# Optimization experiments

Measured on AMD Instinct MI355X. Metric: run time of the kernel, lower is better.

Reference implementation:

```python
import jax, jax.numpy as jnp
import numpy as np

B, NQ, NK, H = 4, 2048, 2048, 512
TEMP = 1.0


def setup_inputs() -> dict:
    key = jax.random.key(0)
    ks = jax.random.split(key, 13)
    s = 0.02
    inp = {
        "query_feat": jax.random.normal(ks[0], (B, NQ, H), jnp.float32),
        "key_feat": jax.random.normal(ks[1], (B, NK, H), jnp.float32),
        "qm_uncert": jax.random.normal(ks[2], (B, NQ), jnp.float32),
        "md_uncert": jax.random.normal(ks[3], (B, NK), jnp.float32),
        "Wq": jax.random.normal(ks[4], (H, H), jnp.float32) * s,
        "bq": jnp.zeros((H,), jnp.float32),
        "Wk": jax.random.normal(ks[5], (H, H), jnp.float32) * s,
        "bk": jnp.zeros((H,), jnp.float32),
        "Wv": jax.random.normal(ks[6], (H, H), jnp.float32) * s,
        "bv": jnp.zeros((H,), jnp.float32),
        "Wo": jax.random.normal(ks[7], (H, H), jnp.float32) * s,
        "bo": jnp.zeros((H,), jnp.float32),
        "tau": jnp.float32(1.0),
    }
    return inp


def reference(query_feat, key_feat, qm_uncert, md_uncert,
              Wq, bq, Wk, bk, Wv, bv, Wo, bo, tau):
    h = query_feat.shape[-1]
    Q = query_feat @ Wq.T + bq          # [B,Nq,H]
    K = key_feat @ Wk.T + bk            # [B,Nk,H]
    V = key_feat @ Wv.T + bv            # [B,Nk,H]

    # scaled dot-product logits
    logits = jnp.einsum('bqh,bkh->bqk', Q, K) / jnp.sqrt(jnp.asarray(h, logits_dtype(Q)))

    # uncertainty weight: sigmoid(tau * (qm_i + md_j)), then sanitize (mult mode)
    u = jax.nn.sigmoid(tau * (qm_uncert[:, :, None] + md_uncert[:, None, :]))
    u = jnp.nan_to_num(u, nan=1.0, posinf=1e6, neginf=1e-6)
    u = jnp.clip(u, 1e-6, 1e6)
    row_sum = jnp.sum(jnp.abs(u), axis=-1, keepdims=True)
    u = jnp.where(row_sum <= 1e-12, jnp.asarray(1e-6, u.dtype), u)

    logits = (logits * u) / TEMP

    # rows fully masked to -1e9 get zeroed (no mask here, but kept for faithfulness)
    all_masked = jnp.all(logits == -1e9, axis=-1, keepdims=True)
    logits = jnp.where(all_masked, jnp.zeros_like(logits), logits)

    attn = jax.nn.softmax(logits, axis=-1)  # dropout p=0 -> identity
    att = jnp.einsum('bqk,bkh->bqh', attn, V)
    out = att @ Wo.T + bo
    return out, attn


def logits_dtype(x):
    return x.dtype
```

## Files before the change

kernel.cpp:

```cpp
#include <hip/hip_runtime.h>
#include <stdint.h>

#define DEVI static __device__ __forceinline__

typedef unsigned short u16;
typedef short bf16x8 __attribute__((ext_vector_type(8)));
typedef u16 u16x8 __attribute__((ext_vector_type(8)));
typedef u16 u16x4 __attribute__((ext_vector_type(4)));
typedef float f32x4 __attribute__((ext_vector_type(4)));

DEVI u16 f2bf(float f) {
    uint32_t u = __builtin_bit_cast(uint32_t, f);
    u += 0x7FFFu + ((u >> 16) & 1u);
    return (u16)(u >> 16);
}
DEVI float bf2f(u16 u) { return __builtin_bit_cast(float, (uint32_t)u << 16); }

struct GemmArgs {
    const void* A;
    const void* A2;
    long long aStrideBytes;
    int lda;
    const u16* Bm;
    long long bStrideElts;
    int ldb;
    int K;
    const float* bias; const float* bias2; const float* bias3;
    u16* outB;
    float* outF;
    long long outFStride;
    const float* qm; const float* md; const float* tauPtr; float scale;
    float* partials;
    u16* vt;
};

enum { EPI_PROJ = 0, EPI_PROJV = 1, EPI_LOGITS = 2, EPI_PV = 3, EPI_OUT = 4,
       EPI_LOGITSB = 5, EPI_PROJ3 = 6 };

template <int EPI, bool AF32>
__global__ __launch_bounds__(256, 2) void gemm_bt(GemmArgs p) {
    __shared__ u16 As[128 * 32];
    __shared__ u16 Bs[128 * 32];
    __shared__ float redBuf[2][128];

    const int tid = threadIdx.x;
    const int lane = tid & 63;
    const int wave = tid >> 6;
    const int g = lane >> 4, lr = lane & 15;
    const int wr = wave >> 1, wc = wave & 1;
    const int z = blockIdx.z;
    const int rowBase = blockIdx.x * 128;
    const int colBase = blockIdx.y * 128;

    int batch = z, koff = 0;
    if constexpr (EPI == EPI_PV) { batch = z & 3; koff = (z >> 2) * p.K; }

    const char* Abase;
    const u16* Bbase;
    const float* bias = p.bias;
    if constexpr (EPI == EPI_PROJ3) {
        Abase = (const char*)(z == 0 ? p.A : p.A2);
        Bbase = p.Bm + (size_t)z * 512 * 512;
        bias = (z == 0) ? p.bias : (z == 1 ? p.bias2 : p.bias3);
    } else {
        Abase = (const char*)p.A + (size_t)batch * p.aStrideBytes + (size_t)koff * (AF32 ? 4 : 2);
        Bbase = p.Bm + (size_t)batch * p.bStrideElts + koff;
    }

    f32x4 acc[4][4] = {};

    const int nk = p.K >> 5;
    for (int kt = 0; kt < nk; ++kt) {
        const int kb = kt << 5;
        float4 areg[4];
        if (AF32) {
            const float* Af = (const float*)Abase;
            const int arow = tid >> 1, kh = (tid & 1) << 4;
            const float* src = Af + (size_t)(rowBase + arow) * p.lda + kb + kh;
            #pragma unroll
            for (int j = 0; j < 4; ++j) areg[j] = ((const float4*)src)[j];
        }
        __syncthreads();
        if (AF32) {
            const int arow = tid >> 1, kh = (tid & 1) << 4;
            u16 tmp[16];
            #pragma unroll
            for (int j = 0; j < 4; ++j) {
                tmp[4 * j + 0] = f2bf(areg[j].x);
                tmp[4 * j + 1] = f2bf(areg[j].y);
                tmp[4 * j + 2] = f2bf(areg[j].z);
                tmp[4 * j + 3] = f2bf(areg[j].w);
            }
            #pragma unroll
            for (int h = 0; h < 2; ++h)
                *(u16x8*)&As[arow * 32 + kh + h * 8] = *(u16x8*)&tmp[h * 8];
        } else {
            #pragma unroll
            for (int i = 0; i < 2; ++i) {
                int c = i * 256 + tid;
                const u16* gp = (const u16*)Abase + (size_t)(rowBase + (c >> 2)) * p.lda + kb + (c & 3) * 8;
                char* lp = (char*)As + (i * 256 + wave * 64) * 16;
                __builtin_amdgcn_global_load_lds((const __attribute__((address_space(1))) void*)gp,
                                                 (__attribute__((address_space(3))) void*)lp, 16, 0, 0);
            }
        }
        #pragma unroll
        for (int i = 0; i < 2; ++i) {
            int c = i * 256 + tid;
            const u16* gp = Bbase + (size_t)(colBase + (c >> 2)) * p.ldb + kb + (c & 3) * 8;
            char* lp = (char*)Bs + (i * 256 + wave * 64) * 16;
            __builtin_amdgcn_global_load_lds((const __attribute__((address_space(1))) void*)gp,
                                             (__attribute__((address_space(3))) void*)lp, 16, 0, 0);
        }
        __syncthreads();

        bf16x8 af[4], bfr[4];
        #pragma unroll
        for (int m = 0; m < 4; ++m)
            af[m] = *(const bf16x8*)&As[(wr * 64 + m * 16 + lr) * 32 + g * 8];
        #pragma unroll
        for (int n = 0; n < 4; ++n)
            bfr[n] = *(const bf16x8*)&Bs[(wc * 64 + n * 16 + lr) * 32 + g * 8];
        #pragma unroll
        for (int m = 0; m < 4; ++m)
            #pragma unroll
            for (int n = 0; n < 4; ++n)
                acc[m][n] = __builtin_amdgcn_mfma_f32_16x16x32_bf16(af[m], bfr[n], acc[m][n], 0, 0, 0);
    }

    const int rB = rowBase + wr * 64;
    const int cB = colBase + wc * 64;

    if constexpr (EPI == EPI_PROJ || EPI == EPI_PROJ3) {
        if (EPI == EPI_PROJ || z < 2) {
            u16* dst = (EPI == EPI_PROJ3) ? p.outB + (size_t)z * 8192 * 512 : p.outB;
            #pragma unroll
            for (int n = 0; n < 4; ++n) {
                int col = cB + n * 16 + lr;
                float bv = bias[col];
                #pragma unroll
                for (int m = 0; m < 4; ++m) {
                    int r0 = rB + m * 16 + g * 4;
                    #pragma unroll
                    for (int i = 0; i < 4; ++i)
                        dst[(size_t)(r0 + i) * 512 + col] = f2bf(acc[m][n][i] + bv);
                }
            }
        } else {
            #pragma unroll
            for (int n = 0; n < 4; ++n) {
                int col = cB + n * 16 + lr;
                float bv = bias[col];
                #pragma unroll
                for (int m = 0; m < 4; ++m) {
                    int r0 = rB + m * 16 + g * 4;
                    int b = r0 >> 11, k0 = r0 & 2047;
                    u16x4 pk;
                    #pragma unroll
                    for (int i = 0; i < 4; ++i) pk[i] = f2bf(acc[m][n][i] + bv);
                    *(u16x4*)&p.vt[((size_t)b * 512 + col) * 2048 + k0] = pk;
                }
            }
        }
    } else if constexpr (EPI == EPI_LOGITS || EPI == EPI_LOGITSB) {
        const float* qmB = p.qm + z * 2048;
        const float* mdB = p.md + z * 2048;
        const float tau = *p.tauPtr;
        float* outRow = p.outF + (size_t)z * p.outFStride;
        float mdv[4];
        #pragma unroll
        for (int n = 0; n < 4; ++n) mdv[n] = mdB[cB + n * 16 + lr];
        #pragma unroll
        for (int m = 0; m < 4; ++m) {
            int r0 = rB + m * 16 + g * 4;
            #pragma unroll
            for (int i = 0; i < 4; ++i) {
                int q = r0 + i;
                float qv = qmB[q];
                float rs = 0.f;
                #pragma unroll
                for (int n = 0; n < 4; ++n) {
                    float t = tau * (qv + mdv[n]);
                    float u = 1.0f / (1.0f + __expf(-t));
                    u = fminf(fmaxf(u, 1e-6f), 1e6f);
                    float e = __expf(acc[m][n][i] * p.scale * u);
                    if (EPI == EPI_LOGITSB)
                        p.outB[((size_t)(z * 2048 + q)) * 2048 + cB + n * 16 + lr] = f2bf(e);
                    else
                        outRow[(size_t)q * 2048 + cB + n * 16 + lr] = e;
                    rs += e;
                }
                #pragma unroll
                for (int off = 1; off < 16; off <<= 1) rs += __shfl_xor(rs, off, 64);
                if (lr == 0) redBuf[wc][wr * 64 + m * 16 + g * 4 + i] = rs;
            }
        }
        __syncthreads();
        if (tid < 128) {
            float s = redBuf[0][tid] + redBuf[1][tid];
            int q = rowBase + tid;
            p.partials[((size_t)z * 2048 + q) * 16 + blockIdx.y] = s;
        }
    } else if constexpr (EPI == EPI_PV) {
        const int split = z >> 2;
        u16* dst = p.outB + (size_t)split * 8192 * 512;
        #pragma unroll
        for (int n = 0; n < 4; ++n) {
            int col = cB + n * 16 + lr;
            #pragma unroll
            for (int m = 0; m < 4; ++m) {
                int r0 = rB + m * 16 + g * 4;
                size_t gr = (size_t)batch * 2048 + r0;
                #pragma unroll
                for (int i = 0; i < 4; ++i)
                    dst[(gr + i) * 512 + col] = f2bf(acc[m][n][i]);
            }
        }
    } else {
        #pragma unroll
        for (int n = 0; n < 4; ++n) {
            int col = cB + n * 16 + lr;
            float bv = p.bias[col];
            #pragma unroll
            for (int m = 0; m < 4; ++m) {
                int r0 = rB + m * 16 + g * 4;
                #pragma unroll
                for (int i = 0; i < 4; ++i)
                    p.outF[(size_t)(r0 + i) * 512 + col] = acc[m][n][i] + bv;
            }
        }
    }
}

__global__ void cvt_weights(const float* a, const float* b, const float* c, const float* d,
                            u16* dst) {
    const float* src;
    switch (blockIdx.y) {
        case 0: src = a; break;
        case 1: src = b; break;
        case 2: src = c; break;
        default: src = d; break;
    }
    int i = (blockIdx.x * 256 + threadIdx.x) * 4;
    float4 v = *(const float4*)(src + i);
    u16x4 u = { f2bf(v.x), f2bf(v.y), f2bf(v.z), f2bf(v.w) };
    *(u16x4*)(dst + (size_t)blockIdx.y * 512 * 512 + i) = u;
}

__global__ void rowsum_inv(const float* __restrict__ partials, float* __restrict__ invs) {
    int r = blockIdx.x * 256 + threadIdx.x;
    float s = 0.f;
    #pragma unroll
    for (int t = 0; t < 16; ++t) s += partials[r * 16 + t];
    invs[r] = 1.0f / s;
}

__global__ void normalize_attn(float* __restrict__ attn, const float* __restrict__ invs) {
    size_t i4 = (size_t)blockIdx.x * 256 + threadIdx.x;
    int row = (int)(i4 >> 9);
    float s = invs[row];
    float4 v = ((const float4*)attn)[i4];
    v.x *= s; v.y *= s; v.z *= s; v.w *= s;
    ((float4*)attn)[i4] = v;
}

__global__ void normalize_bf(const u16* __restrict__ e, float* __restrict__ attn,
                             const float* __restrict__ invs) {
    size_t i8 = (size_t)blockIdx.x * 256 + threadIdx.x;
    size_t e0 = i8 * 8;
    int row = (int)(e0 >> 11);
    float s = invs[row];
    u16x8 v = *(const u16x8*)(e + e0);
    float4 a, b;
    a.x = bf2f(v[0]) * s; a.y = bf2f(v[1]) * s; a.z = bf2f(v[2]) * s; a.w = bf2f(v[3]) * s;
    b.x = bf2f(v[4]) * s; b.y = bf2f(v[5]) * s; b.z = bf2f(v[6]) * s; b.w = bf2f(v[7]) * s;
    ((float4*)(attn + e0))[0] = a;
    ((float4*)(attn + e0))[1] = b;
}

__global__ void pv_reduce(const u16* __restrict__ part, const float* __restrict__ invs,
                          u16* __restrict__ attB) {
    size_t i8 = (size_t)blockIdx.x * 256 + threadIdx.x;
    size_t e0 = i8 * 8;
    int row = (int)(e0 >> 9);
    float s = invs ? invs[row] : 1.0f;
    u16x8 p0 = *(const u16x8*)(part + e0);
    u16x8 p1 = *(const u16x8*)(part + (size_t)8192 * 512 + e0);
    u16x8 o;
    #pragma unroll
    for (int j = 0; j < 8; ++j) o[j] = f2bf((bf2f(p0[j]) + bf2f(p1[j])) * s);
    *(u16x8*)(attB + e0) = o;
}

extern "C" void kernel_launch(void* const* d_in, const int* in_sizes, int n_in,
                              void* d_out, int out_size, void* d_ws, size_t ws_size,
                              hipStream_t stream) {
    const float* qf  = (const float*)d_in[0];
    const float* kf  = (const float*)d_in[1];
    const float* qm  = (const float*)d_in[2];
    const float* md  = (const float*)d_in[3];
    const float* Wq  = (const float*)d_in[4];
    const float* bq  = (const float*)d_in[5];
    const float* Wk  = (const float*)d_in[6];
    const float* bk  = (const float*)d_in[7];
    const float* Wv  = (const float*)d_in[8];
    const float* bv  = (const float*)d_in[9];
    const float* Wo  = (const float*)d_in[10];
    const float* bo  = (const float*)d_in[11];
    const float* tau = (const float*)d_in[12];

    float* out  = (float*)d_out;
    float* attn = out + (size_t)4 * 2048 * 512;

    const size_t NV = (size_t)8192 * 512;
    u16* Qb   = (u16*)d_ws;
    u16* Kb   = Qb + NV;
    u16* Vtb  = Kb + NV;
    u16* Wqb  = Vtb + NV;
    u16* Wob  = Wqb + (size_t)3 * 512 * 512;
    float* partials = (float*)(Wqb + (size_t)4 * 512 * 512);
    float* invs = partials + (size_t)8192 * 16;
    u16* attE = (u16*)(invs + 8192);
    size_t need = (size_t)((char*)(attE + (size_t)4 * 2048 * 2048) - (char*)d_ws);
    const bool big = ws_size >= need;

    u16* partialPV = Qb;
    u16* attB = Vtb;

    dim3 blk(256);
    cvt_weights<<<dim3(256, 4), blk, 0, stream>>>(Wq, Wk, Wv, Wo, Wqb);

    GemmArgs a = {};
    a.A = qf; a.A2 = kf; a.lda = 512; a.ldb = 512; a.K = 512;
    a.Bm = Wqb; a.bias = bq; a.bias2 = bk; a.bias3 = bv;
    a.outB = Qb; a.vt = Vtb;
    gemm_bt<EPI_PROJ3, true><<<dim3(64, 4, 3), blk, 0, stream>>>(a);

    GemmArgs lg = {};
    lg.A = Qb; lg.aStrideBytes = (long long)2048 * 512 * 2; lg.lda = 512;
    lg.Bm = Kb; lg.bStrideElts = (long long)2048 * 512; lg.ldb = 512;
    lg.K = 512;
    lg.qm = qm; lg.md = md; lg.tauPtr = tau;
    lg.scale = 0.04419417382415922f;
    lg.partials = partials;
    if (big) {
        lg.outB = attE;
        gemm_bt<EPI_LOGITSB, false><<<dim3(16, 16, 4), blk, 0, stream>>>(lg);
    } else {
        lg.outF = attn; lg.outFStride = (long long)2048 * 2048;
        gemm_bt<EPI_LOGITS, false><<<dim3(16, 16, 4), blk, 0, stream>>>(lg);
    }

    rowsum_inv<<<dim3(32), blk, 0, stream>>>(partials, invs);

    if (big)
        normalize_bf<<<dim3(8192), blk, 0, stream>>>(attE, attn, invs);
    else
        normalize_attn<<<dim3(16384), blk, 0, stream>>>(attn, invs);

    GemmArgs pv = {};
    pv.Bm = Vtb; pv.bStrideElts = (long long)512 * 2048; pv.ldb = 2048;
    pv.K = 1024; pv.outB = partialPV; pv.lda = 2048;
    if (big) {
        pv.A = attE; pv.aStrideBytes = (long long)2048 * 2048 * 2;
        gemm_bt<EPI_PV, false><<<dim3(16, 4, 8), blk, 0, stream>>>(pv);
        pv_reduce<<<dim3(2048), blk, 0, stream>>>(partialPV, invs, attB);
    } else {
        pv.A = attn; pv.aStrideBytes = (long long)2048 * 2048 * 4;
        gemm_bt<EPI_PV, true><<<dim3(16, 4, 8), blk, 0, stream>>>(pv);
        pv_reduce<<<dim3(2048), blk, 0, stream>>>(partialPV, nullptr, attB);
    }

    GemmArgs og = {};
    og.A = attB; og.lda = 512;
    og.Bm = Wob; og.ldb = 512;
    og.K = 512; og.bias = bo; og.outF = out;
    gemm_bt<EPI_OUT, false><<<dim3(64, 4, 1), blk, 0, stream>>>(og);
}
```

Baseline: 143.3 us.

## Fuse attn normalization into PV grid and split-K reduction into output GEMM

Removes the separate normalize_bf and pv_reduce kernels. The bf16-to-fp32 normalized attention write is done by extra blocks (blockIdx.y==4) inside the PV GEMM launch, so it runs alongside the matmul. The output projection now loads both split-K partial PV buffers, sums and scales them by the inverse row sum while staging A into LDS, and uses a 64-row tile to keep the grid larger. This saves two launches and one round trip of the intermediate through memory, at the cost of heavier A staging in the output GEMM and uneven work across blocks in the PV grid.

```diff
diff --git a/kernel.cpp b/kernel.cpp
--- a/kernel.cpp
+++ b/kernel.cpp
@@ -31,15 +31,16 @@
     long long outFStride;
     const float* qm; const float* md; const float* tauPtr; float scale;
     float* partials;
+    const float* invsPtr;
     u16* vt;
 };
 
-enum { EPI_PROJ = 0, EPI_PROJV = 1, EPI_LOGITS = 2, EPI_PV = 3, EPI_OUT = 4,
-       EPI_LOGITSB = 5, EPI_PROJ3 = 6 };
-
-template <int EPI, bool AF32>
+enum { EPI_PROJ3 = 0, EPI_LOGITS = 1, EPI_LOGITSB = 2, EPI_PV = 3, EPI_OUT = 4 };
+
+template <int EPI, int AMODE, int TM>
 __global__ __launch_bounds__(256, 2) void gemm_bt(GemmArgs p) {
-    __shared__ u16 As[128 * 32];
+    constexpr int NF = (TM == 128) ? 4 : 2;
+    __shared__ u16 As[TM * 32];
     __shared__ u16 Bs[128 * 32];
     __shared__ float redBuf[2][128];
 
@@ -47,9 +48,10 @@
     const int lane = tid & 63;
     const int wave = tid >> 6;
     const int g = lane >> 4, lr = lane & 15;
-    const int wr = wave >> 1, wc = wave & 1;
+    const int waveRowBase = (TM == 128) ? (wave >> 1) * 64 : 0;
+    const int waveColBase = (TM == 128) ? (wave & 1) * 64 : wave * 32;
     const int z = blockIdx.z;
-    const int rowBase = blockIdx.x * 128;
+    const int rowBase = blockIdx.x * TM;
     const int colBase = blockIdx.y * 128;
 
     int batch = z, koff = 0;
@@ -63,25 +65,61 @@
         Bbase = p.Bm + (size_t)z * 512 * 512;
         bias = (z == 0) ? p.bias : (z == 1 ? p.bias2 : p.bias3);
     } else {
-        Abase = (const char*)p.A + (size_t)batch * p.aStrideBytes + (size_t)koff * (AF32 ? 4 : 2);
+        Abase = (const char*)p.A + (size_t)batch * p.aStrideBytes + (size_t)koff * (AMODE == 1 ? 4 : 2);
         Bbase = p.Bm + (size_t)batch * p.bStrideElts + koff;
     }
 
-    f32x4 acc[4][4] = {};
+    if constexpr (EPI == EPI_PV && AMODE == 0) {
+        if (blockIdx.y == 4) {
+            const u16* e = (const u16*)Abase + (size_t)rowBase * 2048;
+            float* attnOut = p.outF + (size_t)batch * p.outFStride + (size_t)rowBase * 2048 + koff;
+            const float* invs = p.invsPtr + batch * 2048 + rowBase;
+            #pragma unroll 4
+            for (int it = 0; it < 64; ++it) {
+                int cc = it * 256 + tid;
+                int row = cc >> 7, colc = (cc & 127) * 8;
+                float s = invs[row];
+                u16x8 v = *(const u16x8*)(e + (size_t)row * 2048 + colc);
+                float4 f0, f1;
+                f0.x = bf2f(v[0]) * s; f0.y = bf2f(v[1]) * s;
+                f0.z = bf2f(v[2]) * s; f0.w = bf2f(v[3]) * s;
+                f1.x = bf2f(v[4]) * s; f1.y = bf2f(v[5]) * s;
+                f1.z = bf2f(v[6]) * s; f1.w = bf2f(v[7]) * s;
+                float* dst = attnOut + (size_t)row * 2048 + colc;
+                ((float4*)dst)[0] = f0;
+                ((float4*)dst)[1] = f1;
+            }
+            return;
+        }
+    }
+
+    f32x4 acc[4][NF] = {};
+
+    const int arow2 = tid >> 2, kh2 = (tid & 3) << 3;
+    const u16* pa0 = nullptr; const u16* pa1 = nullptr; float sInv = 1.0f;
+    if constexpr (AMODE == 2) {
+        pa0 = (const u16*)p.A + (size_t)(rowBase + arow2) * 512 + kh2;
+        pa1 = pa0 + (size_t)8192 * 512;
+        sInv = p.invsPtr ? p.invsPtr[rowBase + arow2] : 1.0f;
+    }
 
     const int nk = p.K >> 5;
     for (int kt = 0; kt < nk; ++kt) {
         const int kb = kt << 5;
         float4 areg[4];
-        if (AF32) {
+        u16x8 a0, a1;
+        if constexpr (AMODE == 1) {
             const float* Af = (const float*)Abase;
             const int arow = tid >> 1, kh = (tid & 1) << 4;
             const float* src = Af + (size_t)(rowBase + arow) * p.lda + kb + kh;
             #pragma unroll
             for (int j = 0; j < 4; ++j) areg[j] = ((const float4*)src)[j];
+        } else if constexpr (AMODE == 2) {
+            a0 = *(const u16x8*)(pa0 + kb);
+            a1 = *(const u16x8*)(pa1 + kb);
         }
         __syncthreads();
-        if (AF32) {
+        if constexpr (AMODE == 1) {
             const int arow = tid >> 1, kh = (tid & 1) << 4;
             u16 tmp[16];
             #pragma unroll
@@ -94,9 +132,15 @@
             #pragma unroll
             for (int h = 0; h < 2; ++h)
                 *(u16x8*)&As[arow * 32 + kh + h * 8] = *(u16x8*)&tmp[h * 8];
+        } else if constexpr (AMODE == 2) {
+            u16 tmp[8];
+            #pragma unroll
+            for (int j = 0; j < 8; ++j)
+                tmp[j] = f2bf((bf2f(a0[j]) + bf2f(a1[j])) * sInv);
+            *(u16x8*)&As[arow2 * 32 + kh2] = *(u16x8*)tmp;
         } else {
             #pragma unroll
-            for (int i = 0; i < 2; ++i) {
+            for (int i = 0; i < TM / 64; ++i) {
                 int c = i * 256 + tid;
                 const u16* gp = (const u16*)Abase + (size_t)(rowBase + (c >> 2)) * p.lda + kb + (c & 3) * 8;
                 char* lp = (char*)As + (i * 256 + wave * 64) * 16;
@@ -114,28 +158,28 @@
         }
         __syncthreads();
 
-        bf16x8 af[4], bfr[4];
+        bf16x8 af[4], bfr[NF];
         #pragma unroll
         for (int m = 0; m < 4; ++m)
-            af[m] = *(const bf16x8*)&As[(wr * 64 + m * 16 + lr) * 32 + g * 8];
-        #pragma unroll
-        for (int n = 0; n < 4; ++n)
-            bfr[n] = *(const bf16x8*)&Bs[(wc * 64 + n * 16 + lr) * 32 + g * 8];
+            af[m] = *(const bf16x8*)&As[(waveRowBase + m * 16 + lr) * 32 + g * 8];
+        #pragma unroll
+        for (int n = 0; n < NF; ++n)
+            bfr[n] = *(const bf16x8*)&Bs[(waveColBase + n * 16 + lr) * 32 + g * 8];
         #pragma unroll
         for (int m = 0; m < 4; ++m)
             #pragma unroll
-            for (int n = 0; n < 4; ++n)
+            for (int n = 0; n < NF; ++n)
                 acc[m][n] = __builtin_amdgcn_mfma_f32_16x16x32_bf16(af[m], bfr[n], acc[m][n], 0, 0, 0);
     }
 
-    const int rB = rowBase + wr * 64;
-    const int cB = colBase + wc * 64;
-
-    if constexpr (EPI == EPI_PROJ || EPI == EPI_PROJ3) {
-        if (EPI == EPI_PROJ || z < 2) {
-            u16* dst = (EPI == EPI_PROJ3) ? p.outB + (size_t)z * 8192 * 512 : p.outB;
-            #pragma unroll
-            for (int n = 0; n < 4; ++n) {
+    const int rB = rowBase + waveRowBase;
+    const int cB = colBase + waveColBase;
+
+    if constexpr (EPI == EPI_PROJ3) {
+        if (z < 2) {
+            u16* dst = p.outB + (size_t)z * 8192 * 512;
+            #pragma unroll
+            for (int n = 0; n < NF; ++n) {
                 int col = cB + n * 16 + lr;
                 float bv = bias[col];
                 #pragma unroll
@@ -148,7 +192,7 @@
             }
         } else {
             #pragma unroll
-            for (int n = 0; n < 4; ++n) {
+            for (int n = 0; n < NF; ++n) {
                 int col = cB + n * 16 + lr;
                 float bv = bias[col];
                 #pragma unroll
@@ -167,9 +211,9 @@
         const float* mdB = p.md + z * 2048;
         const float tau = *p.tauPtr;
         float* outRow = p.outF + (size_t)z * p.outFStride;
-        float mdv[4];
-        #pragma unroll
-        for (int n = 0; n < 4; ++n) mdv[n] = mdB[cB + n * 16 + lr];
+        float mdv[NF];
+        #pragma unroll
+        for (int n = 0; n < NF; ++n) mdv[n] = mdB[cB + n * 16 + lr];
         #pragma unroll
         for (int m = 0; m < 4; ++m) {
             int r0 = rB + m * 16 + g * 4;
@@ -179,7 +223,7 @@
                 float qv = qmB[q];
                 float rs = 0.f;
                 #pragma unroll
-                for (int n = 0; n < 4; ++n) {
+                for (int n = 0; n < NF; ++n) {
                     float t = tau * (qv + mdv[n]);
                     float u = 1.0f / (1.0f + __expf(-t));
                     u = fminf(fmaxf(u, 1e-6f), 1e6f);
@@ -192,7 +236,7 @@
                 }
                 #pragma unroll
                 for (int off = 1; off < 16; off <<= 1) rs += __shfl_xor(rs, off, 64);
-                if (lr == 0) redBuf[wc][wr * 64 + m * 16 + g * 4 + i] = rs;
+                if (lr == 0) redBuf[wave & 1][waveRowBase + m * 16 + g * 4 + i] = rs;
             }
         }
         __syncthreads();
@@ -205,7 +249,7 @@
         const int split = z >> 2;
         u16* dst = p.outB + (size_t)split * 8192 * 512;
         #pragma unroll
-        for (int n = 0; n < 4; ++n) {
+        for (int n = 0; n < NF; ++n) {
             int col = cB + n * 16 + lr;
             #pragma unroll
             for (int m = 0; m < 4; ++m) {
@@ -218,7 +262,7 @@
         }
     } else {
         #pragma unroll
-        for (int n = 0; n < 4; ++n) {
+        for (int n = 0; n < NF; ++n) {
             int col = cB + n * 16 + lr;
             float bv = p.bias[col];
             #pragma unroll
@@ -262,34 +306,6 @@
     float4 v = ((const float4*)attn)[i4];
     v.x *= s; v.y *= s; v.z *= s; v.w *= s;
     ((float4*)attn)[i4] = v;
-}
-
-__global__ void normalize_bf(const u16* __restrict__ e, float* __restrict__ attn,
-                             const float* __restrict__ invs) {
-    size_t i8 = (size_t)blockIdx.x * 256 + threadIdx.x;
-    size_t e0 = i8 * 8;
-    int row = (int)(e0 >> 11);
-    float s = invs[row];
-    u16x8 v = *(const u16x8*)(e + e0);
-    float4 a, b;
-    a.x = bf2f(v[0]) * s; a.y = bf2f(v[1]) * s; a.z = bf2f(v[2]) * s; a.w = bf2f(v[3]) * s;
-    b.x = bf2f(v[4]) * s; b.y = bf2f(v[5]) * s; b.z = bf2f(v[6]) * s; b.w = bf2f(v[7]) * s;
-    ((float4*)(attn + e0))[0] = a;
-    ((float4*)(attn + e0))[1] = b;
-}
-
-__global__ void pv_reduce(const u16* __restrict__ part, const float* __restrict__ invs,
-                          u16* __restrict__ attB) {
-    size_t i8 = (size_t)blockIdx.x * 256 + threadIdx.x;
-    size_t e0 = i8 * 8;
-    int row = (int)(e0 >> 9);
-    float s = invs ? invs[row] : 1.0f;
-    u16x8 p0 = *(const u16x8*)(part + e0);
-    u16x8 p1 = *(const u16x8*)(part + (size_t)8192 * 512 + e0);
-    u16x8 o;
-    #pragma unroll
-    for (int j = 0; j < 8; ++j) o[j] = f2bf((bf2f(p0[j]) + bf2f(p1[j])) * s);
-    *(u16x8*)(attB + e0) = o;
 }
 
 extern "C" void kernel_launch(void* const* d_in, const int* in_sizes, int n_in,
@@ -325,7 +341,6 @@
     const bool big = ws_size >= need;
 
     u16* partialPV = Qb;
-    u16* attB = Vtb;
 
     dim3 blk(256);
     cvt_weights<<<dim3(256, 4), blk, 0, stream>>>(Wq, Wk, Wv, Wo, Wqb);
@@ -334,7 +349,7 @@
     a.A = qf; a.A2 = kf; a.lda = 512; a.ldb = 512; a.K = 512;
     a.Bm = Wqb; a.bias = bq; a.bias2 = bk; a.bias3 = bv;
     a.outB = Qb; a.vt = Vtb;
-    gemm_bt<EPI_PROJ3, true><<<dim3(64, 4, 3), blk, 0, stream>>>(a);
+    gemm_bt<EPI_PROJ3, 1, 128><<<dim3(64, 4, 3), blk, 0, stream>>>(a);
 
     GemmArgs lg = {};
     lg.A = Qb; lg.aStrideBytes = (long long)2048 * 512 * 2; lg.lda = 512;
@@ -345,35 +360,32 @@
     lg.partials = partials;
     if (big) {
         lg.outB = attE;
-        gemm_bt<EPI_LOGITSB, false><<<dim3(16, 16, 4), blk, 0, stream>>>(lg);
+        gemm_bt<EPI_LOGITSB, 0, 128><<<dim3(16, 16, 4), blk, 0, stream>>>(lg);
     } else {
         lg.outF = attn; lg.outFStride = (long long)2048 * 2048;
-        gemm_bt<EPI_LOGITS, false><<<dim3(16, 16, 4), blk, 0, stream>>>(lg);
+        gemm_bt<EPI_LOGITS, 0, 128><<<dim3(16, 16, 4), blk, 0, stream>>>(lg);
     }
 
     rowsum_inv<<<dim3(32), blk, 0, stream>>>(partials, invs);
-
-    if (big)
-        normalize_bf<<<dim3(8192), blk, 0, stream>>>(attE, attn, invs);
-    else
-        normalize_attn<<<dim3(16384), blk, 0, stream>>>(attn, invs);
 
     GemmArgs pv = {};
     pv.Bm = Vtb; pv.bStrideElts = (long long)512 * 2048; pv.ldb = 2048;
     pv.K = 1024; pv.outB = partialPV; pv.lda = 2048;
+    pv.invsPtr = invs;
     if (big) {
         pv.A = attE; pv.aStrideBytes = (long long)2048 * 2048 * 2;
-        gemm_bt<EPI_PV, false><<<dim3(16, 4, 8), blk, 0, stream>>>(pv);
-        pv_reduce<<<dim3(2048), blk, 0, stream>>>(partialPV, invs, attB);
+        pv.outF = attn; pv.outFStride = (long long)2048 * 2048;
+        gemm_bt<EPI_PV, 0, 128><<<dim3(16, 5, 8), blk, 0, stream>>>(pv);
     } else {
+        normalize_attn<<<dim3(16384), blk, 0, stream>>>(attn, invs);
         pv.A = attn; pv.aStrideBytes = (long long)2048 * 2048 * 4;
-        gemm_bt<EPI_PV, true><<<dim3(16, 4, 8), blk, 0, stream>>>(pv);
-        pv_reduce<<<dim3(2048), blk, 0, stream>>>(partialPV, nullptr, attB);
+        gemm_bt<EPI_PV, 1, 128><<<dim3(16, 4, 8), blk, 0, stream>>>(pv);
     }
 
     GemmArgs og = {};
-    og.A = attB; og.lda = 512;
+    og.A = partialPV; og.lda = 512;
     og.Bm = Wob; og.ldb = 512;
     og.K = 512; og.bias = bo; og.outF = out;
-    gemm_bt<EPI_OUT, false><<<dim3(64, 4, 1), blk, 0, stream>>>(og);
-}
+    og.invsPtr = big ? invs : nullptr;
+    gemm_bt<EPI_OUT, 2, 64><<<dim3(128, 4, 1), blk, 0, stream>>>(og);
+}
```

Measured after the change: 132.1 us. -7.8%, faster.
